# Kernel tuning notes

Measured on AMD Instinct MI355X. Metric: run time of the kernel, lower is better.

## Reference

```python
import jax, jax.numpy as jnp
import numpy as np

N_ITERATIONS = 3  # matches init_kwargs n_iterations


def squash(s):
    # s: [batch, output_caps, output_dim]
    sq = jnp.sum(s * s, axis=2, keepdims=True)          # [b, oc, 1]
    return s * (sq / (1.0 + sq) / jnp.sqrt(sq))


def setup_inputs() -> dict:
    key = jax.random.key(0)
    k_u, = jax.random.split(key, 1)
    batch, ic, oc, od = 128, 2048, 32, 16
    u_predict = jax.random.normal(k_u, (batch, ic, oc, od), dtype=jnp.float32)
    b = jnp.zeros((ic, oc), dtype=jnp.float32)  # routing logit prior, init zeros per torch module
    return {"u_predict": u_predict, "b": b}


def reference(u_predict, b):
    # u_predict: [batch, input_caps, output_caps, output_dim]; b: [input_caps, output_caps]
    batch = u_predict.shape[0]
    c = jax.nn.softmax(b, axis=1)                              # softmax over output_caps (torch implicit dim=1 on 2D)
    s = jnp.einsum('io,biod->bod', c, u_predict)               # weighted sum over input_caps
    v = squash(s)
    b_batch = jnp.broadcast_to(b, (batch,) + b.shape)          # [b, ic, oc]
    for _ in range(N_ITERATIONS):
        b_batch = b_batch + jnp.einsum('biod,bod->bio', u_predict, v)  # agreement
        c = jax.nn.softmax(b_batch, axis=-1)                   # coupling coeffs over output_caps
        s = jnp.einsum('bio,biod->bod', c, u_predict)
        v = squash(s)
    return v
```

## Files before the change

kernel.cpp:

```cpp
#include <hip/hip_runtime.h>
#include <math.h>


namespace {
constexpr int BATCH = 128;
constexpr int IC    = 2048;
constexpr int OC    = 32;
constexpr int OD    = 16;
constexpr int ROW   = OC * OD;
constexpr int BPB   = 16;
constexpr int ROWS_PER_BLOCK = IC / BPB;
constexpr int NWAVES = 4;
}

__device__ __forceinline__ float dot8(const float4& a0, const float4& a1,
                                      const float4& b0, const float4& b1) {
    return a0.x*b0.x + a0.y*b0.y + a0.z*b0.z + a0.w*b0.w
         + a1.x*b1.x + a1.y*b1.y + a1.z*b1.z + a1.w*b1.w;
}

template<int NV>
__global__ void __launch_bounds__(256)
routing_pass(const float* __restrict__ u,
             const float* __restrict__ blogit,
             const float* __restrict__ sbuf,
             float* __restrict__ s_out)
{
    const int tid   = threadIdx.x;
    const int lane  = tid & 63;
    const int wave  = tid >> 6;
    const int b     = blockIdx.x / BPB;
    const int chunk = blockIdx.x % BPB;
    const int i0    = chunk * ROWS_PER_BLOCK;

    const int o     = lane >> 1;
    const int elem0 = lane * 8;

    float4 v0[NV > 0 ? NV : 1];
    float4 v1[NV > 0 ? NV : 1];
#pragma unroll
    for (int t = 0; t < NV; ++t) {
        const float* sp = sbuf + ((size_t)t * BATCH + b) * ROW + elem0;
        float4 x0 = *(const float4*)sp;
        float4 x1 = *(const float4*)(sp + 4);
        float part = x0.x*x0.x + x0.y*x0.y + x0.z*x0.z + x0.w*x0.w
                   + x1.x*x1.x + x1.y*x1.y + x1.z*x1.z + x1.w*x1.w;
        float sq = part + __shfl_xor(part, 1, 64);
        float scale = sqrtf(sq) / (1.0f + sq);
        x0.x *= scale; x0.y *= scale; x0.z *= scale; x0.w *= scale;
        x1.x *= scale; x1.y *= scale; x1.z *= scale; x1.w *= scale;
        v0[t] = x0; v1[t] = x1;
    }

    float4 acc0 = make_float4(0.f, 0.f, 0.f, 0.f);
    float4 acc1 = make_float4(0.f, 0.f, 0.f, 0.f);

    for (int i = i0 + wave; i < i0 + ROWS_PER_BLOCK; i += NWAVES) {
        const float* urow = u + ((size_t)b * IC + i) * ROW + elem0;
        float4 u0 = *(const float4*)urow;
        float4 u1 = *(const float4*)(urow + 4);

        float bb = blogit[i * OC + o];
#pragma unroll
        for (int t = 0; t < NV; ++t) {
            float part = dot8(u0, u1, v0[t], v1[t]);
            bb += part + __shfl_xor(part, 1, 64);
        }

        float m = bb;
#pragma unroll
        for (int off = 2; off <= 32; off <<= 1)
            m = fmaxf(m, __shfl_xor(m, off, 64));
        float e = __expf(bb - m);
        float ssum = e;
#pragma unroll
        for (int off = 2; off <= 32; off <<= 1)
            ssum += __shfl_xor(ssum, off, 64);
        const float c = e / ssum;

        acc0.x += c * u0.x; acc0.y += c * u0.y; acc0.z += c * u0.z; acc0.w += c * u0.w;
        acc1.x += c * u1.x; acc1.y += c * u1.y; acc1.z += c * u1.z; acc1.w += c * u1.w;
    }

    __shared__ float red[NWAVES * ROW];
    float* my = red + wave * ROW + elem0;
    *(float4*)my       = acc0;
    *(float4*)(my + 4) = acc1;
    __syncthreads();

    float* dst = s_out + (size_t)b * ROW;
    for (int p = tid; p < ROW; p += 256) {
        float val = red[p] + red[ROW + p] + red[2 * ROW + p] + red[3 * ROW + p];
        atomicAdd(dst + p, val);
    }
}

__global__ void __launch_bounds__(256)
squash_out(const float* __restrict__ s, float* __restrict__ out)
{
    const int idx = blockIdx.x * 256 + threadIdx.x;
    const float x = s[idx];
    float p = x * x;
    p += __shfl_xor(p, 1, 64);
    p += __shfl_xor(p, 2, 64);
    p += __shfl_xor(p, 4, 64);
    p += __shfl_xor(p, 8, 64);
    const float scale = sqrtf(p) / (1.0f + p);
    out[idx] = x * scale;
}

extern "C" void kernel_launch(void* const* d_in, const int* in_sizes, int n_in,
                              void* d_out, int out_size, void* d_ws, size_t ws_size,
                              hipStream_t stream)
{
    const float* u  = (const float*)d_in[0];
    const float* bl = (const float*)d_in[1];
    float* out  = (float*)d_out;
    float* sbuf = (float*)d_ws;

    constexpr size_t SSZ = (size_t)BATCH * ROW;

    hipMemsetAsync(sbuf, 0, 4 * SSZ * sizeof(float), stream);

    dim3 grid(BATCH * BPB), block(256);
    routing_pass<0><<<grid, block, 0, stream>>>(u, bl, sbuf, sbuf + 0 * SSZ);
    routing_pass<1><<<grid, block, 0, stream>>>(u, bl, sbuf, sbuf + 1 * SSZ);
    routing_pass<2><<<grid, block, 0, stream>>>(u, bl, sbuf, sbuf + 2 * SSZ);
    routing_pass<3><<<grid, block, 0, stream>>>(u, bl, sbuf, sbuf + 3 * SSZ);
    squash_out<<<dim3((BATCH * ROW) / 256), block, 0, stream>>>(sbuf + 3 * SSZ, out);
}
```

Before: 984.4 us.

## Cache u in fp16 once, sum squashed outputs, and reduce partials without atomics

The first pass does the initial weighted sum from fp32 u and also writes an fp16 copy of u. The three routing iterations then read that half-size copy instead of the fp32 tensor. Squashed outputs are accumulated into one running vector w, so each iteration needs a single dot product per row instead of one per previous iteration. Per-block partials are written out and reduced by a separate squash kernel, replacing atomics and the memset; the softmax max-subtraction is dropped and loads are software-prefetched. This costs an extra 268MB write plus fp16 rounding error in u, and unshifted exp could overflow for large logits.

```diff
diff --git a/kernel.cpp b/kernel.cpp
--- a/kernel.cpp
+++ b/kernel.cpp
@@ -11,102 +11,153 @@
 constexpr int BPB   = 16;
 constexpr int ROWS_PER_BLOCK = IC / BPB;
 constexpr int NWAVES = 4;
+
+typedef _Float16 half8 __attribute__((ext_vector_type(8)));
+typedef float    f32x4 __attribute__((ext_vector_type(4)));
+
+constexpr size_t OFF_U16  = 0;
+constexpr size_t OFF_PART = 268435456;
+constexpr size_t OFF_W    = OFF_PART + 4194304;
+constexpr size_t OFF_C0   = OFF_W + 262144;
 }
 
-__device__ __forceinline__ float dot8(const float4& a0, const float4& a1,
-                                      const float4& b0, const float4& b1) {
-    return a0.x*b0.x + a0.y*b0.y + a0.z*b0.z + a0.w*b0.w
-         + a1.x*b1.x + a1.y*b1.y + a1.z*b1.z + a1.w*b1.w;
+__global__ void __launch_bounds__(256)
+softmax_b(const float* __restrict__ blogit, float* __restrict__ c0)
+{
+    const int idx = blockIdx.x * 256 + threadIdx.x;
+    float x = blogit[idx];
+    float m = x;
+#pragma unroll
+    for (int off = 1; off <= 16; off <<= 1)
+        m = fmaxf(m, __shfl_xor(m, off, 64));
+    float e = __expf(x - m);
+    float s = e;
+#pragma unroll
+    for (int off = 1; off <= 16; off <<= 1)
+        s += __shfl_xor(s, off, 64);
+    c0[idx] = e / s;
 }
 
-template<int NV>
 __global__ void __launch_bounds__(256)
-routing_pass(const float* __restrict__ u,
-             const float* __restrict__ blogit,
-             const float* __restrict__ sbuf,
-             float* __restrict__ s_out)
+pass0_convert(const float* __restrict__ u, const float* __restrict__ c0,
+              _Float16* __restrict__ u16, float* __restrict__ partials)
 {
-    const int tid   = threadIdx.x;
-    const int lane  = tid & 63;
-    const int wave  = tid >> 6;
-    const int b     = blockIdx.x / BPB;
-    const int chunk = blockIdx.x % BPB;
-    const int i0    = chunk * ROWS_PER_BLOCK;
+    const int tid = threadIdx.x, lane = tid & 63, wave = tid >> 6;
+    const int b = blockIdx.x >> 4, chunk = blockIdx.x & 15;
+    const int o = lane >> 1, elem0 = lane * 8;
+    const int i_base = chunk * ROWS_PER_BLOCK + wave * 32;
 
-    const int o     = lane >> 1;
-    const int elem0 = lane * 8;
+    f32x4 acc0 = {0.f,0.f,0.f,0.f}, acc1 = {0.f,0.f,0.f,0.f};
 
-    float4 v0[NV > 0 ? NV : 1];
-    float4 v1[NV > 0 ? NV : 1];
-#pragma unroll
-    for (int t = 0; t < NV; ++t) {
-        const float* sp = sbuf + ((size_t)t * BATCH + b) * ROW + elem0;
-        float4 x0 = *(const float4*)sp;
-        float4 x1 = *(const float4*)(sp + 4);
-        float part = x0.x*x0.x + x0.y*x0.y + x0.z*x0.z + x0.w*x0.w
-                   + x1.x*x1.x + x1.y*x1.y + x1.z*x1.z + x1.w*x1.w;
-        float sq = part + __shfl_xor(part, 1, 64);
-        float scale = sqrtf(sq) / (1.0f + sq);
-        x0.x *= scale; x0.y *= scale; x0.z *= scale; x0.w *= scale;
-        x1.x *= scale; x1.y *= scale; x1.z *= scale; x1.w *= scale;
-        v0[t] = x0; v1[t] = x1;
-    }
+    const float*  ubase = u   + ((size_t)b * IC + i_base) * ROW + elem0;
+    _Float16*     obase = u16 + ((size_t)b * IC + i_base) * ROW + elem0;
 
-    float4 acc0 = make_float4(0.f, 0.f, 0.f, 0.f);
-    float4 acc1 = make_float4(0.f, 0.f, 0.f, 0.f);
-
-    for (int i = i0 + wave; i < i0 + ROWS_PER_BLOCK; i += NWAVES) {
-        const float* urow = u + ((size_t)b * IC + i) * ROW + elem0;
-        float4 u0 = *(const float4*)urow;
-        float4 u1 = *(const float4*)(urow + 4);
-
-        float bb = blogit[i * OC + o];
-#pragma unroll
-        for (int t = 0; t < NV; ++t) {
-            float part = dot8(u0, u1, v0[t], v1[t]);
-            bb += part + __shfl_xor(part, 1, 64);
-        }
-
-        float m = bb;
-#pragma unroll
-        for (int off = 2; off <= 32; off <<= 1)
-            m = fmaxf(m, __shfl_xor(m, off, 64));
-        float e = __expf(bb - m);
-        float ssum = e;
-#pragma unroll
-        for (int off = 2; off <= 32; off <<= 1)
-            ssum += __shfl_xor(ssum, off, 64);
-        const float c = e / ssum;
-
-        acc0.x += c * u0.x; acc0.y += c * u0.y; acc0.z += c * u0.z; acc0.w += c * u0.w;
-        acc1.x += c * u1.x; acc1.y += c * u1.y; acc1.z += c * u1.z; acc1.w += c * u1.w;
+#pragma unroll 4
+    for (int r = 0; r < 32; ++r) {
+        const float* up = ubase + (size_t)r * ROW;
+        f32x4 u0 = __builtin_nontemporal_load((const f32x4*)up);
+        f32x4 u1 = __builtin_nontemporal_load((const f32x4*)(up + 4));
+        float c = c0[(i_base + r) * OC + o];
+        acc0 += c * u0;
+        acc1 += c * u1;
+        half8 h;
+        h[0]=(_Float16)u0[0]; h[1]=(_Float16)u0[1]; h[2]=(_Float16)u0[2]; h[3]=(_Float16)u0[3];
+        h[4]=(_Float16)u1[0]; h[5]=(_Float16)u1[1]; h[6]=(_Float16)u1[2]; h[7]=(_Float16)u1[3];
+        __builtin_nontemporal_store(h, (half8*)(obase + (size_t)r * ROW));
     }
 
     __shared__ float red[NWAVES * ROW];
     float* my = red + wave * ROW + elem0;
-    *(float4*)my       = acc0;
-    *(float4*)(my + 4) = acc1;
+    *(f32x4*)my       = acc0;
+    *(f32x4*)(my + 4) = acc1;
     __syncthreads();
-
-    float* dst = s_out + (size_t)b * ROW;
-    for (int p = tid; p < ROW; p += 256) {
-        float val = red[p] + red[ROW + p] + red[2 * ROW + p] + red[3 * ROW + p];
-        atomicAdd(dst + p, val);
-    }
+    float* dst = partials + (size_t)blockIdx.x * ROW;
+    for (int p = tid; p < ROW; p += 256)
+        dst[p] = red[p] + red[ROW + p] + red[2*ROW + p] + red[3*ROW + p];
 }
 
 __global__ void __launch_bounds__(256)
-squash_out(const float* __restrict__ s, float* __restrict__ out)
+pass_iter(const _Float16* __restrict__ u16, const float* __restrict__ blogit,
+          const float* __restrict__ w, float* __restrict__ partials)
+{
+    const int tid = threadIdx.x, lane = tid & 63, wave = tid >> 6;
+    const int b = blockIdx.x >> 4, chunk = blockIdx.x & 15;
+    const int o = lane >> 1, elem0 = lane * 8;
+    const int i_base = chunk * ROWS_PER_BLOCK + wave * 32;
+
+    const float* wp = w + (size_t)b * ROW + elem0;
+    const f32x4 w0 = *(const f32x4*)wp;
+    const f32x4 w1 = *(const f32x4*)(wp + 4);
+
+    f32x4 acc0 = {0.f,0.f,0.f,0.f}, acc1 = {0.f,0.f,0.f,0.f};
+
+    const half8* ubase = (const half8*)(u16 + ((size_t)b * IC + i_base) * ROW + elem0);
+
+    half8 cur[4];
+    cur[0] = ubase[0*64]; cur[1] = ubase[1*64]; cur[2] = ubase[2*64]; cur[3] = ubase[3*64];
+
+    for (int g = 0; g < 8; ++g) {
+        half8 nxt[4];
+        if (g < 7) {
+            const half8* p = ubase + (size_t)(g + 1) * 4 * 64;
+            nxt[0] = p[0*64]; nxt[1] = p[1*64]; nxt[2] = p[2*64]; nxt[3] = p[3*64];
+        }
+        float blg[4];
+#pragma unroll
+        for (int r = 0; r < 4; ++r)
+            blg[r] = blogit[(i_base + g*4 + r) * OC + o];
+
+#pragma unroll
+        for (int r = 0; r < 4; ++r) {
+            float uf[8];
+#pragma unroll
+            for (int j = 0; j < 8; ++j) uf[j] = (float)cur[r][j];
+            float part = uf[0]*w0[0] + uf[1]*w0[1] + uf[2]*w0[2] + uf[3]*w0[3]
+                       + uf[4]*w1[0] + uf[5]*w1[1] + uf[6]*w1[2] + uf[7]*w1[3];
+            float bb = blg[r] + part + __shfl_xor(part, 1, 64);
+            float e = __expf(bb);
+            float ssum = e;
+#pragma unroll
+            for (int off = 2; off <= 32; off <<= 1)
+                ssum += __shfl_xor(ssum, off, 64);
+            const float c = e / ssum;
+            acc0[0] += c*uf[0]; acc0[1] += c*uf[1]; acc0[2] += c*uf[2]; acc0[3] += c*uf[3];
+            acc1[0] += c*uf[4]; acc1[1] += c*uf[5]; acc1[2] += c*uf[6]; acc1[3] += c*uf[7];
+        }
+#pragma unroll
+        for (int r = 0; r < 4; ++r) cur[r] = nxt[r];
+    }
+
+    __shared__ float red[NWAVES * ROW];
+    float* my = red + wave * ROW + elem0;
+    *(f32x4*)my       = acc0;
+    *(f32x4*)(my + 4) = acc1;
+    __syncthreads();
+    float* dst = partials + (size_t)blockIdx.x * ROW;
+    for (int p = tid; p < ROW; p += 256)
+        dst[p] = red[p] + red[ROW + p] + red[2*ROW + p] + red[3*ROW + p];
+}
+
+template<int MODE>
+__global__ void __launch_bounds__(256)
+reduce_squash(const float* __restrict__ partials, float* __restrict__ w,
+              float* __restrict__ out)
 {
     const int idx = blockIdx.x * 256 + threadIdx.x;
-    const float x = s[idx];
-    float p = x * x;
-    p += __shfl_xor(p, 1, 64);
-    p += __shfl_xor(p, 2, 64);
-    p += __shfl_xor(p, 4, 64);
-    p += __shfl_xor(p, 8, 64);
-    const float scale = sqrtf(p) / (1.0f + p);
-    out[idx] = x * scale;
+    const int b = idx >> 9, p = idx & 511;
+    const float* pp = partials + (size_t)(b * BPB) * ROW + p;
+    float s = 0.f;
+#pragma unroll
+    for (int k = 0; k < BPB; ++k) s += pp[k * ROW];
+    float sq = s * s;
+    sq += __shfl_xor(sq, 1, 64);
+    sq += __shfl_xor(sq, 2, 64);
+    sq += __shfl_xor(sq, 4, 64);
+    sq += __shfl_xor(sq, 8, 64);
+    const float v = s * (sqrtf(sq) / (1.0f + sq));
+    if (MODE == 0)      w[idx] = v;
+    else if (MODE == 1) w[idx] += v;
+    else                out[idx] = v;
 }
 
 extern "C" void kernel_launch(void* const* d_in, const int* in_sizes, int n_in,
@@ -115,17 +166,25 @@
 {
     const float* u  = (const float*)d_in[0];
     const float* bl = (const float*)d_in[1];
-    float* out  = (float*)d_out;
-    float* sbuf = (float*)d_ws;
+    float* out = (float*)d_out;
 
-    constexpr size_t SSZ = (size_t)BATCH * ROW;
+    char* ws = (char*)d_ws;
+    _Float16* u16     = (_Float16*)(ws + OFF_U16);
+    float*    partials= (float*)(ws + OFF_PART);
+    float*    wbuf    = (float*)(ws + OFF_W);
+    float*    c0      = (float*)(ws + OFF_C0);
 
-    hipMemsetAsync(sbuf, 0, 4 * SSZ * sizeof(float), stream);
+    const dim3 blk(256);
+    const dim3 gpass(BATCH * BPB);
+    const dim3 gred(BATCH * ROW / 256);
 
-    dim3 grid(BATCH * BPB), block(256);
-    routing_pass<0><<<grid, block, 0, stream>>>(u, bl, sbuf, sbuf + 0 * SSZ);
-    routing_pass<1><<<grid, block, 0, stream>>>(u, bl, sbuf, sbuf + 1 * SSZ);
-    routing_pass<2><<<grid, block, 0, stream>>>(u, bl, sbuf, sbuf + 2 * SSZ);
-    routing_pass<3><<<grid, block, 0, stream>>>(u, bl, sbuf, sbuf + 3 * SSZ);
-    squash_out<<<dim3((BATCH * ROW) / 256), block, 0, stream>>>(sbuf + 3 * SSZ, out);
+    softmax_b   <<<dim3(IC * OC / 256), blk, 0, stream>>>(bl, c0);
+    pass0_convert<<<gpass, blk, 0, stream>>>(u, c0, u16, partials);
+    reduce_squash<0><<<gred, blk, 0, stream>>>(partials, wbuf, out);
+    pass_iter   <<<gpass, blk, 0, stream>>>(u16, bl, wbuf, partials);
+    reduce_squash<1><<<gred, blk, 0, stream>>>(partials, wbuf, out);
+    pass_iter   <<<gpass, blk, 0, stream>>>(u16, bl, wbuf, partials);
+    reduce_squash<1><<<gred, blk, 0, stream>>>(partials, wbuf, out);
+    pass_iter   <<<gpass, blk, 0, stream>>>(u16, bl, wbuf, partials);
+    reduce_squash<2><<<gred, blk, 0, stream>>>(partials, wbuf, out);
 }
```

Result: faster. 856.6 us (-13.0%).
